# Optimization experiments

Measured on AMD Instinct MI355X. Metric: run time of the kernel, lower is better.

The kernel has to match this reference:

```python
import jax, jax.numpy as jnp
import numpy as np

HEADS = 8
DIM_HEAD = 64


def setup_inputs() -> dict:
    key = jax.random.key(0)
    k1, k2, k3 = jax.random.split(key, 3)
    b, hw, n, dim = 2, 1024, 64, 512
    x = jax.random.normal(k1, (b, hw, n, dim), dtype=jnp.float32)
    w_qkv = jax.random.normal(k2, (3 * HEADS * DIM_HEAD, dim), dtype=jnp.float32) * 0.02
    pos_bias = jax.random.normal(k3, (HEADS, n, n), dtype=jnp.float32)
    # one batch attends everywhere, one focuses on the present frame (eye mask)
    focus_present_mask = jnp.arange(b).astype(bool)
    return {"x": x, "w_qkv": w_qkv, "pos_bias": pos_bias,
            "focus_present_mask": focus_present_mask}


def reference(x, w_qkv, pos_bias, focus_present_mask):
    b, hw, n, dim = x.shape
    h, d = HEADS, DIM_HEAD
    scale = d ** -0.5

    # fused qkv projection (no bias)
    qkv = jnp.einsum('bsnc,ec->bsne', x, w_qkv)          # (b, hw, n, 3*h*d)
    q, k, v = jnp.split(qkv, 3, axis=-1)

    def to_heads(t):  # '... n (h d) -> ... h n d'
        return jnp.moveaxis(t.reshape(b, hw, n, h, d), 3, 2)

    q, k, v = map(to_heads, (q, k, v))                   # (b, hw, h, n, d)
    q = q * scale

    sim = jnp.einsum('bshid,bshjd->bshij', q, k)         # (b, hw, h, n, n)
    sim = sim + pos_bias                                 # broadcast (h, n, n)

    # focus-present mask: eye for focused batches, all-ones otherwise
    eye = jnp.eye(n, dtype=bool)
    ones = jnp.ones((n, n), dtype=bool)
    mask = jnp.where(focus_present_mask[:, None, None, None, None],
                     eye[None, None, None], ones[None, None, None])  # (b,1,1,n,n)
    neg_max = -jnp.finfo(sim.dtype).max
    sim = jnp.where(mask, sim, neg_max)

    attn = jax.nn.softmax(sim, axis=-1)                  # includes the amax shift
    out = jnp.einsum('bshij,bshjd->bshid', attn, v)      # (b, hw, h, n, d)
    out = jnp.moveaxis(out, 2, 3).reshape(b, hw, n, h * d)  # '... h n d -> ... n (h d)'
    return out
```

## Files before the change

kernel.cpp:

```cpp
#include <hip/hip_runtime.h>
#include <hip/hip_bf16.h>


typedef __attribute__((ext_vector_type(4))) float f32x4;
typedef __attribute__((ext_vector_type(8))) short s16x8;

#define DIM 512

__device__ __forceinline__ short f2bf(float f) {
    __hip_bfloat16 h = __float2bfloat16(f);
    return __builtin_bit_cast(short, h);
}
__device__ __forceinline__ f32x4 ntld4(const float* p) {
    return __builtin_nontemporal_load((const f32x4*)p);
}
__device__ __forceinline__ void ntst4(float* p, f32x4 v) {
    __builtin_nontemporal_store(v, (f32x4*)p);
}
__device__ __forceinline__ s16x8 pack8(f32x4 a, f32x4 b) {
    s16x8 v;
    v[0] = f2bf(a[0]); v[1] = f2bf(a[1]); v[2] = f2bf(a[2]); v[3] = f2bf(a[3]);
    v[4] = f2bf(b[0]); v[5] = f2bf(b[1]); v[6] = f2bf(b[2]); v[7] = f2bf(b[3]);
    return v;
}
__device__ __forceinline__ int xaddr(int row, int kb) {
    return (row << 10) + (kb ^ ((row & 7) << 4));
}
__device__ __forceinline__ int taddr(int row, int kb) {
    return (row << 7) + (kb ^ ((row & 7) << 4));
}

__global__ void conv_w(const float* __restrict__ w, unsigned short* __restrict__ wb) {
    int gid  = blockIdx.x * 256 + threadIdx.x;
    int lane = gid & 63;
    int ks   = (gid >> 6) & 15;
    int rowblk = gid >> 10;
    int row = rowblk * 16 + (lane & 15);
    int col = ks * 32 + (lane >> 4) * 8;
    const float* p = w + (size_t)row * DIM + col;
    f32x4 a = *(const f32x4*)p;
    f32x4 b = *(const f32x4*)(p + 4);
    float sc = (row < 512) ? 0.125f : 1.0f;
    a *= sc; b *= sc;
    *(s16x8*)(wb + (size_t)gid * 8) = pack8(a, b);
}

template<int WB16>
__device__ __forceinline__ s16x8 wfragL(const unsigned short* __restrict__ wb,
                                        const float* __restrict__ w,
                                        int rowblk, int ks, int lane) {
    if constexpr (WB16) {
        return *(const s16x8*)(wb + ((size_t)(rowblk * 16 + ks) * 64 + lane) * 8);
    } else {
        int row = rowblk * 16 + (lane & 15);
        int col = ks * 32 + (lane >> 4) * 8;
        const float* p = w + (size_t)row * DIM + col;
        f32x4 u0 = *(const f32x4*)p;
        f32x4 u1 = *(const f32x4*)(p + 4);
        float sc = (row < 512) ? 0.125f : 1.0f;
        u0 *= sc; u1 *= sc;
        return pack8(u0, u1);
    }
}

__device__ __forceinline__ bool decode_mask(const unsigned int* mk, int b) {
    unsigned int m0 = mk[0], m1 = mk[1];
    if (m0 <= 1u && m1 <= 1u) return ((b == 0) ? m0 : m1) != 0u;
    return ((const unsigned char*)mk)[b] != 0;
}

#define MFB(a, b, cc) __builtin_amdgcn_mfma_f32_16x16x32_bf16(a, b, cc, 0, 0, 0)
#define PRIO1 __builtin_amdgcn_s_setprio(1);
#define PRIO0 __builtin_amdgcn_s_setprio(0);

#define XF(ks)                                                               \
    s16x8 af0 = *(const s16x8*)(smem + xaddr(c,      (ks) * 64 + g * 16));   \
    s16x8 af1 = *(const s16x8*)(smem + xaddr(16 + c, (ks) * 64 + g * 16));   \
    s16x8 af2 = *(const s16x8*)(smem + xaddr(32 + c, (ks) * 64 + g * 16));   \
    s16x8 af3 = *(const s16x8*)(smem + xaddr(48 + c, (ks) * 64 + g * 16));

template<int WB16>
__global__ __launch_bounds__(1024, 4)
void attn_merged(const float* __restrict__ x,
                 const float* __restrict__ w,
                 const unsigned short* __restrict__ wb,
                 const float* __restrict__ pb,
                 const unsigned int* __restrict__ mk,
                 float* __restrict__ out)
{
    extern __shared__ char smem[];
    const int tid  = threadIdx.x;
    const int lane = tid & 63;
    const int wave = tid >> 6;
    const int g    = lane >> 4;
    const int c    = lane & 15;
    const int hp   = wave >> 1;
    const int hw2  = wave & 1;
    const int site = blockIdx.x;
    const bool focused = decode_mask(mk, site >> 10);
    const float* xblk   = x   + (size_t)site * (64 * DIM);
    float*       outblk = out + (size_t)site * (64 * DIM);
    const f32x4 zf = {0.f, 0.f, 0.f, 0.f};

    {
        const int row = tid >> 4, c16 = tid & 15;
        const float* gp = xblk + row * DIM;
        #pragma unroll
        for (int j = 0; j < 4; ++j) {
            f32x4 a = ntld4(gp + j * 128 + c16 * 8);
            f32x4 b = ntld4(gp + j * 128 + c16 * 8 + 4);
            *(s16x8*)(smem + xaddr(row, j * 256 + c16 * 16)) = pack8(a, b);
        }
    }
    __syncthreads();

    if (focused) {
        const int RB = 64 + hp * 4 + 2 * hw2;
        f32x4 va[2][4];
        #pragma unroll
        for (int i = 0; i < 2; ++i)
            #pragma unroll
            for (int j = 0; j < 4; ++j) va[i][j] = zf;
        #pragma unroll 4
        for (int ks = 0; ks < 16; ++ks) {
            s16x8 wv0 = wfragL<WB16>(wb, w, RB,     ks, lane);
            s16x8 wv1 = wfragL<WB16>(wb, w, RB + 1, ks, lane);
            XF(ks)
            PRIO1
            va[0][0]=MFB(wv0,af0,va[0][0]); va[0][1]=MFB(wv0,af1,va[0][1]);
            va[0][2]=MFB(wv0,af2,va[0][2]); va[0][3]=MFB(wv0,af3,va[0][3]);
            va[1][0]=MFB(wv1,af0,va[1][0]); va[1][1]=MFB(wv1,af1,va[1][1]);
            va[1][2]=MFB(wv1,af2,va[1][2]); va[1][3]=MFB(wv1,af3,va[1][3]);
            PRIO0
        }
        char* stg = smem + 65536;
        #pragma unroll
        for (int h2 = 0; h2 < 2; ++h2) {
            #pragma unroll
            for (int sub = 0; sub < 2; ++sub)
                #pragma unroll
                for (int tn = 0; tn < 2; ++tn) {
                    int rl   = tn * 16 + c;
                    int colb = hp * 256 + hw2 * 128 + sub * 64 + g * 16;
                    *(f32x4*)(stg + rl * 2048 + (colb ^ ((rl & 7) << 4))) =
                        va[sub][h2 * 2 + tn];
                }
            __syncthreads();
            #pragma unroll
            for (int i = 0; i < 4; ++i) {
                int lin = i * 16384 + tid * 16;
                int rl = lin >> 11, off = lin & 2047;
                f32x4 v = *(const f32x4*)(stg + rl * 2048 + (off ^ ((rl & 7) << 4)));
                ntst4((float*)((char*)outblk + h2 * 65536 + lin), v);
            }
            if (h2 == 0) __syncthreads();
        }
        return;
    }

    char* slotA = smem + hp * 8192;
    char* slotB = smem + 65536 + hp * 8192;
    const int RQ = hp * 4 + 2 * hw2;
    const int RK = 32 + hp * 4 + 2 * hw2;

    {
        f32x4 acc[4][2];
        #pragma unroll
        for (int t = 0; t < 4; ++t) { acc[t][0] = zf; acc[t][1] = zf; }
        #pragma unroll 4
        for (int ks = 0; ks < 16; ++ks) {
            s16x8 w0 = wfragL<WB16>(wb, w, RQ,     ks, lane);
            s16x8 w1 = wfragL<WB16>(wb, w, RQ + 1, ks, lane);
            XF(ks)
            PRIO1
            acc[0][0]=MFB(af0,w0,acc[0][0]); acc[0][1]=MFB(af0,w1,acc[0][1]);
            acc[1][0]=MFB(af1,w0,acc[1][0]); acc[1][1]=MFB(af1,w1,acc[1][1]);
            acc[2][0]=MFB(af2,w0,acc[2][0]); acc[2][1]=MFB(af2,w1,acc[2][1]);
            acc[3][0]=MFB(af3,w0,acc[3][0]); acc[3][1]=MFB(af3,w1,acc[3][1]);
            PRIO0
        }
        #pragma unroll
        for (int t = 0; t < 4; ++t)
            #pragma unroll
            for (int hc = 0; hc < 2; ++hc)
                #pragma unroll
                for (int rr = 0; rr < 4; ++rr) {
                    int row = t * 16 + g * 4 + rr;
                    int col = hw2 * 32 + hc * 16 + c;
                    *(short*)(slotB + (row << 7) + ((col * 2) ^ ((row & 7) << 4))) =
                        f2bf(acc[t][hc][rr]);
                }
    }

    s16x8 kc[4];
    {
        f32x4 acc[4][2];
        #pragma unroll
        for (int t = 0; t < 4; ++t) { acc[t][0] = zf; acc[t][1] = zf; }
        #pragma unroll 4
        for (int ks = 0; ks < 16; ++ks) {
            s16x8 w0 = wfragL<WB16>(wb, w, RK,     ks, lane);
            s16x8 w1 = wfragL<WB16>(wb, w, RK + 1, ks, lane);
            XF(ks)
            PRIO1
            acc[0][0]=MFB(af0,w0,acc[0][0]); acc[0][1]=MFB(af0,w1,acc[0][1]);
            acc[1][0]=MFB(af1,w0,acc[1][0]); acc[1][1]=MFB(af1,w1,acc[1][1]);
            acc[2][0]=MFB(af2,w0,acc[2][0]); acc[2][1]=MFB(af2,w1,acc[2][1]);
            acc[3][0]=MFB(af3,w0,acc[3][0]); acc[3][1]=MFB(af3,w1,acc[3][1]);
            PRIO0
        }
        #pragma unroll
        for (int t = 0; t < 4; ++t) kc[t] = pack8(acc[t][0], acc[t][1]);
    }

    s16x8 vc[4];
    #pragma unroll
    for (int sub = 0; sub < 2; ++sub) {
        const int RB = 64 + hp * 4 + 2 * hw2 + sub;
        f32x4 a0 = zf, a1 = zf, a2 = zf, a3 = zf;
        #pragma unroll 4
        for (int ks = 0; ks < 16; ++ks) {
            s16x8 wv = wfragL<WB16>(wb, w, RB, ks, lane);
            XF(ks)
            PRIO1
            a0 = MFB(wv, af0, a0); a1 = MFB(wv, af1, a1);
            a2 = MFB(wv, af2, a2); a3 = MFB(wv, af3, a3);
            PRIO0
        }
        vc[sub * 2]     = pack8(a0, a1);
        vc[sub * 2 + 1] = pack8(a2, a3);
    }

    __syncthreads();

    #pragma unroll
    for (int t = 0; t < 4; ++t)
        #pragma unroll
        for (int hc = 0; hc < 2; ++hc)
            #pragma unroll
            for (int rr = 0; rr < 4; ++rr) {
                int row = t * 16 + g * 4 + rr;
                int col = hw2 * 32 + hc * 16 + c;
                *(short*)(slotA + (row << 7) + ((col * 2) ^ ((row & 7) << 4))) =
                    kc[t][hc * 4 + rr];
            }
    __syncthreads();

    s16x8 qf[2][2];
    #pragma unroll
    for (int ks2 = 0; ks2 < 2; ++ks2)
        #pragma unroll
        for (int tr2 = 0; tr2 < 2; ++tr2)
            qf[ks2][tr2] = *(const s16x8*)(slotB +
                taddr((2 * hw2 + tr2) * 16 + c, ks2 * 64 + g * 16));

    #pragma unroll
    for (int sub = 0; sub < 2; ++sub)
        #pragma unroll
        for (int t = 0; t < 4; ++t)
            #pragma unroll
            for (int rr = 0; rr < 4; ++rr) {
                int row = hw2 * 32 + sub * 16 + g * 4 + rr;
                int col = t * 16 + c;
                *(short*)(slotB + (row << 7) + ((col * 2) ^ ((row & 7) << 4))) =
                    vc[sub * 2 + (t >> 1)][(t & 1) * 4 + rr];
            }

    f32x4 sm[2][4];
    #pragma unroll
    for (int i = 0; i < 2; ++i)
        #pragma unroll
        for (int j = 0; j < 4; ++j) sm[i][j] = zf;
    #pragma unroll
    for (int ks2 = 0; ks2 < 2; ++ks2) {
        #pragma unroll
        for (int j = 0; j < 4; ++j) {
            s16x8 bk = *(const s16x8*)(slotA + taddr(j * 16 + c, ks2 * 64 + g * 16));
            PRIO1
            sm[0][j] = MFB(qf[ks2][0], bk, sm[0][j]);
            sm[1][j] = MFB(qf[ks2][1], bk, sm[1][j]);
            PRIO0
        }
    }

    const float* pbh = pb + hp * 4096;
    #pragma unroll
    for (int tr = 0; tr < 2; ++tr) {
        #pragma unroll
        for (int rr = 0; rr < 4; ++rr) {
            const int i = 32 * hw2 + tr * 16 + g * 4 + rr;
            float v0 = sm[tr][0][rr] + pbh[i * 64 +  0 + c];
            float v1 = sm[tr][1][rr] + pbh[i * 64 + 16 + c];
            float v2 = sm[tr][2][rr] + pbh[i * 64 + 32 + c];
            float v3 = sm[tr][3][rr] + pbh[i * 64 + 48 + c];
            float mx = fmaxf(fmaxf(v0, v1), fmaxf(v2, v3));
            mx = fmaxf(mx, __shfl_xor(mx, 1));
            mx = fmaxf(mx, __shfl_xor(mx, 2));
            mx = fmaxf(mx, __shfl_xor(mx, 4));
            mx = fmaxf(mx, __shfl_xor(mx, 8));
            float p0 = __expf(v0 - mx);
            float p1 = __expf(v1 - mx);
            float p2 = __expf(v2 - mx);
            float p3 = __expf(v3 - mx);
            float ssum = p0 + p1 + p2 + p3;
            ssum += __shfl_xor(ssum, 1);
            ssum += __shfl_xor(ssum, 2);
            ssum += __shfl_xor(ssum, 4);
            ssum += __shfl_xor(ssum, 8);
            float rinv = 1.0f / ssum;
            sm[tr][0][rr] = p0 * rinv; sm[tr][1][rr] = p1 * rinv;
            sm[tr][2][rr] = p2 * rinv; sm[tr][3][rr] = p3 * rinv;
        }
    }
    __syncthreads();

    #pragma unroll
    for (int tr = 0; tr < 2; ++tr)
        #pragma unroll
        for (int tc = 0; tc < 4; ++tc)
            #pragma unroll
            for (int rr = 0; rr < 4; ++rr) {
                int row = 32 * hw2 + tr * 16 + g * 4 + rr;
                int col = tc * 16 + c;
                *(short*)(slotA + (row << 7) + ((col * 2) ^ ((row & 7) << 4))) =
                    f2bf(sm[tr][tc][rr]);
            }

    f32x4 ot[4][2];
    #pragma unroll
    for (int i = 0; i < 4; ++i) { ot[i][0] = zf; ot[i][1] = zf; }
    #pragma unroll
    for (int ks2 = 0; ks2 < 2; ++ks2) {
        s16x8 ba0 = *(const s16x8*)(slotA + taddr((2 * hw2 + 0) * 16 + c, ks2 * 64 + g * 16));
        s16x8 ba1 = *(const s16x8*)(slotA + taddr((2 * hw2 + 1) * 16 + c, ks2 * 64 + g * 16));
        #pragma unroll
        for (int i = 0; i < 4; ++i) {
            s16x8 av = *(const s16x8*)(slotB + taddr(i * 16 + c, ks2 * 64 + g * 16));
            PRIO1
            ot[i][0] = MFB(av, ba0, ot[i][0]);
            ot[i][1] = MFB(av, ba1, ot[i][1]);
            PRIO0
        }
    }
    __syncthreads();

    #pragma unroll
    for (int i = 0; i < 4; ++i)
        #pragma unroll
        for (int j = 0; j < 2; ++j) {
            int rl   = 32 * hw2 + j * 16 + c;
            int colb = hp * 256 + i * 64 + g * 16;
            *(f32x4*)(smem + rl * 2048 + (colb ^ ((rl & 7) << 4))) = ot[i][j];
        }
    __syncthreads();
    #pragma unroll
    for (int i = 0; i < 8; ++i) {
        int lin = i * 16384 + tid * 16;
        int rl = lin >> 11, off = lin & 2047;
        f32x4 v = *(const f32x4*)(smem + rl * 2048 + (off ^ ((rl & 7) << 4)));
        ntst4((float*)((char*)outblk + lin), v);
    }
}

extern "C" void kernel_launch(void* const* d_in, const int* in_sizes, int n_in,
                              void* d_out, int out_size, void* d_ws, size_t ws_size,
                              hipStream_t stream)
{
    const float* x  = (const float*)d_in[0];
    const float* w  = (const float*)d_in[1];
    const float* pb = (const float*)d_in[2];
    const unsigned int* mk = (const unsigned int*)d_in[3];
    float* out = (float*)d_out;

    const int LDS = 131072;
    const size_t wbytes = (size_t)1536 * 512 * sizeof(unsigned short);

    if (ws_size >= wbytes) {
        unsigned short* wbp = (unsigned short*)d_ws;
        conv_w<<<dim3(384), dim3(256), 0, stream>>>(w, wbp);
        hipFuncSetAttribute(reinterpret_cast<const void*>(&attn_merged<1>),
                            hipFuncAttributeMaxDynamicSharedMemorySize, LDS);
        attn_merged<1><<<dim3(2048), dim3(1024), LDS, stream>>>(x, w, wbp, pb, mk, out);
    } else {
        hipFuncSetAttribute(reinterpret_cast<const void*>(&attn_merged<0>),
                            hipFuncAttributeMaxDynamicSharedMemorySize, LDS);
        attn_merged<0><<<dim3(2048), dim3(1024), LDS, stream>>>(x, w, nullptr, pb, mk, out);
    }
}
```

Before: 262.1 us.

## Split QKV projection across waves by token rows instead of head columns

Each wave pair now computes its half of the 64 tokens against all four weight row-blocks, rather than all tokens against half the output columns. This halves the shared-memory X fragment reads per k-step but doubles the per-wave weight fragment loads. The write-back layouts for Q, K and V, and the barrier placement, are reorganized to match. The likely motivation is lower LDS traffic, at the cost of more global or L2 weight traffic and more registers.

```diff
diff --git a/kernel.cpp b/kernel.cpp
--- a/kernel.cpp
+++ b/kernel.cpp
@@ -78,6 +78,10 @@
     s16x8 af1 = *(const s16x8*)(smem + xaddr(16 + c, (ks) * 64 + g * 16));   \
     s16x8 af2 = *(const s16x8*)(smem + xaddr(32 + c, (ks) * 64 + g * 16));   \
     s16x8 af3 = *(const s16x8*)(smem + xaddr(48 + c, (ks) * 64 + g * 16));
+
+#define XH(ks)                                                               \
+    s16x8 ax0 = *(const s16x8*)(smem + xaddr(hw2 * 32 + c,      (ks) * 64 + g * 16)); \
+    s16x8 ax1 = *(const s16x8*)(smem + xaddr(hw2 * 32 + 16 + c, (ks) * 64 + g * 16));
 
 template<int WB16>
 __global__ __launch_bounds__(1024, 4)
@@ -160,91 +164,101 @@
 
     char* slotA = smem + hp * 8192;
     char* slotB = smem + 65536 + hp * 8192;
-    const int RQ = hp * 4 + 2 * hw2;
-    const int RK = 32 + hp * 4 + 2 * hw2;
+    const int RQ0 = hp * 4;
+    const int RK0 = 32 + hp * 4;
+    const int RV0 = 64 + hp * 4;
 
     {
-        f32x4 acc[4][2];
-        #pragma unroll
-        for (int t = 0; t < 4; ++t) { acc[t][0] = zf; acc[t][1] = zf; }
+        f32x4 acc[2][4];
+        #pragma unroll
+        for (int i = 0; i < 2; ++i)
+            #pragma unroll
+            for (int j = 0; j < 4; ++j) acc[i][j] = zf;
         #pragma unroll 4
         for (int ks = 0; ks < 16; ++ks) {
-            s16x8 w0 = wfragL<WB16>(wb, w, RQ,     ks, lane);
-            s16x8 w1 = wfragL<WB16>(wb, w, RQ + 1, ks, lane);
-            XF(ks)
-            PRIO1
-            acc[0][0]=MFB(af0,w0,acc[0][0]); acc[0][1]=MFB(af0,w1,acc[0][1]);
-            acc[1][0]=MFB(af1,w0,acc[1][0]); acc[1][1]=MFB(af1,w1,acc[1][1]);
-            acc[2][0]=MFB(af2,w0,acc[2][0]); acc[2][1]=MFB(af2,w1,acc[2][1]);
-            acc[3][0]=MFB(af3,w0,acc[3][0]); acc[3][1]=MFB(af3,w1,acc[3][1]);
-            PRIO0
-        }
-        #pragma unroll
-        for (int t = 0; t < 4; ++t)
-            #pragma unroll
-            for (int hc = 0; hc < 2; ++hc)
+            s16x8 w0 = wfragL<WB16>(wb, w, RQ0,     ks, lane);
+            s16x8 w1 = wfragL<WB16>(wb, w, RQ0 + 1, ks, lane);
+            s16x8 w2 = wfragL<WB16>(wb, w, RQ0 + 2, ks, lane);
+            s16x8 w3 = wfragL<WB16>(wb, w, RQ0 + 3, ks, lane);
+            XH(ks)
+            PRIO1
+            acc[0][0]=MFB(ax0,w0,acc[0][0]); acc[0][1]=MFB(ax0,w1,acc[0][1]);
+            acc[0][2]=MFB(ax0,w2,acc[0][2]); acc[0][3]=MFB(ax0,w3,acc[0][3]);
+            acc[1][0]=MFB(ax1,w0,acc[1][0]); acc[1][1]=MFB(ax1,w1,acc[1][1]);
+            acc[1][2]=MFB(ax1,w2,acc[1][2]); acc[1][3]=MFB(ax1,w3,acc[1][3]);
+            PRIO0
+        }
+        #pragma unroll
+        for (int t2 = 0; t2 < 2; ++t2)
+            #pragma unroll
+            for (int d = 0; d < 4; ++d)
                 #pragma unroll
                 for (int rr = 0; rr < 4; ++rr) {
-                    int row = t * 16 + g * 4 + rr;
-                    int col = hw2 * 32 + hc * 16 + c;
+                    int row = hw2 * 32 + t2 * 16 + g * 4 + rr;
+                    int col = d * 16 + c;
                     *(short*)(slotB + (row << 7) + ((col * 2) ^ ((row & 7) << 4))) =
-                        f2bf(acc[t][hc][rr]);
+                        f2bf(acc[t2][d][rr]);
                 }
     }
 
     s16x8 kc[4];
     {
-        f32x4 acc[4][2];
-        #pragma unroll
-        for (int t = 0; t < 4; ++t) { acc[t][0] = zf; acc[t][1] = zf; }
+        f32x4 acc[2][4];
+        #pragma unroll
+        for (int i = 0; i < 2; ++i)
+            #pragma unroll
+            for (int j = 0; j < 4; ++j) acc[i][j] = zf;
         #pragma unroll 4
         for (int ks = 0; ks < 16; ++ks) {
-            s16x8 w0 = wfragL<WB16>(wb, w, RK,     ks, lane);
-            s16x8 w1 = wfragL<WB16>(wb, w, RK + 1, ks, lane);
-            XF(ks)
-            PRIO1
-            acc[0][0]=MFB(af0,w0,acc[0][0]); acc[0][1]=MFB(af0,w1,acc[0][1]);
-            acc[1][0]=MFB(af1,w0,acc[1][0]); acc[1][1]=MFB(af1,w1,acc[1][1]);
-            acc[2][0]=MFB(af2,w0,acc[2][0]); acc[2][1]=MFB(af2,w1,acc[2][1]);
-            acc[3][0]=MFB(af3,w0,acc[3][0]); acc[3][1]=MFB(af3,w1,acc[3][1]);
-            PRIO0
-        }
-        #pragma unroll
-        for (int t = 0; t < 4; ++t) kc[t] = pack8(acc[t][0], acc[t][1]);
+            s16x8 w0 = wfragL<WB16>(wb, w, RK0,     ks, lane);
+            s16x8 w1 = wfragL<WB16>(wb, w, RK0 + 1, ks, lane);
+            s16x8 w2 = wfragL<WB16>(wb, w, RK0 + 2, ks, lane);
+            s16x8 w3 = wfragL<WB16>(wb, w, RK0 + 3, ks, lane);
+            XH(ks)
+            PRIO1
+            acc[0][0]=MFB(ax0,w0,acc[0][0]); acc[0][1]=MFB(ax0,w1,acc[0][1]);
+            acc[0][2]=MFB(ax0,w2,acc[0][2]); acc[0][3]=MFB(ax0,w3,acc[0][3]);
+            acc[1][0]=MFB(ax1,w0,acc[1][0]); acc[1][1]=MFB(ax1,w1,acc[1][1]);
+            acc[1][2]=MFB(ax1,w2,acc[1][2]); acc[1][3]=MFB(ax1,w3,acc[1][3]);
+            PRIO0
+        }
+        kc[0] = pack8(acc[0][0], acc[0][1]);
+        kc[1] = pack8(acc[0][2], acc[0][3]);
+        kc[2] = pack8(acc[1][0], acc[1][1]);
+        kc[3] = pack8(acc[1][2], acc[1][3]);
     }
 
     s16x8 vc[4];
     #pragma unroll
     for (int sub = 0; sub < 2; ++sub) {
-        const int RB = 64 + hp * 4 + 2 * hw2 + sub;
-        f32x4 a0 = zf, a1 = zf, a2 = zf, a3 = zf;
+        f32x4 a00 = zf, a01 = zf, a10 = zf, a11 = zf;
         #pragma unroll 4
         for (int ks = 0; ks < 16; ++ks) {
-            s16x8 wv = wfragL<WB16>(wb, w, RB, ks, lane);
-            XF(ks)
-            PRIO1
-            a0 = MFB(wv, af0, a0); a1 = MFB(wv, af1, a1);
-            a2 = MFB(wv, af2, a2); a3 = MFB(wv, af3, a3);
-            PRIO0
-        }
-        vc[sub * 2]     = pack8(a0, a1);
-        vc[sub * 2 + 1] = pack8(a2, a3);
-    }
-
-    __syncthreads();
-
-    #pragma unroll
-    for (int t = 0; t < 4; ++t)
-        #pragma unroll
-        for (int hc = 0; hc < 2; ++hc)
+            s16x8 wv0 = wfragL<WB16>(wb, w, RV0 + 2 * sub,     ks, lane);
+            s16x8 wv1 = wfragL<WB16>(wb, w, RV0 + 2 * sub + 1, ks, lane);
+            XH(ks)
+            PRIO1
+            a00 = MFB(wv0, ax0, a00); a01 = MFB(wv0, ax1, a01);
+            a10 = MFB(wv1, ax0, a10); a11 = MFB(wv1, ax1, a11);
+            PRIO0
+        }
+        vc[sub * 2]     = pack8(a00, a01);
+        vc[sub * 2 + 1] = pack8(a10, a11);
+    }
+
+    __syncthreads();
+
+    #pragma unroll
+    for (int t2 = 0; t2 < 2; ++t2)
+        #pragma unroll
+        for (int d = 0; d < 4; ++d)
             #pragma unroll
             for (int rr = 0; rr < 4; ++rr) {
-                int row = t * 16 + g * 4 + rr;
-                int col = hw2 * 32 + hc * 16 + c;
+                int row = hw2 * 32 + t2 * 16 + g * 4 + rr;
+                int col = d * 16 + c;
                 *(short*)(slotA + (row << 7) + ((col * 2) ^ ((row & 7) << 4))) =
-                    kc[t][hc * 4 + rr];
+                    kc[t2 * 2 + (d >> 1)][(d & 1) * 4 + rr];
             }
-    __syncthreads();
 
     s16x8 qf[2][2];
     #pragma unroll
@@ -254,16 +268,18 @@
             qf[ks2][tr2] = *(const s16x8*)(slotB +
                 taddr((2 * hw2 + tr2) * 16 + c, ks2 * 64 + g * 16));
 
-    #pragma unroll
-    for (int sub = 0; sub < 2; ++sub)
-        #pragma unroll
-        for (int t = 0; t < 4; ++t)
+    __syncthreads();
+
+    #pragma unroll
+    for (int i = 0; i < 4; ++i)
+        #pragma unroll
+        for (int t2 = 0; t2 < 2; ++t2)
             #pragma unroll
             for (int rr = 0; rr < 4; ++rr) {
-                int row = hw2 * 32 + sub * 16 + g * 4 + rr;
-                int col = t * 16 + c;
+                int row = i * 16 + g * 4 + rr;
+                int col = hw2 * 32 + t2 * 16 + c;
                 *(short*)(slotB + (row << 7) + ((col * 2) ^ ((row & 7) << 4))) =
-                    vc[sub * 2 + (t >> 1)][(t & 1) * 4 + rr];
+                    vc[i][t2 * 4 + rr];
             }
 
     f32x4 sm[2][4];
```

New measurement: 272.7 us. +4.0%, slower.
